# Optimization experiments

Hardware: AMD Instinct MI355X
Metric: run time of the kernel (lower is better)

Reference implementation:

```python
import jax, jax.numpy as jnp
import numpy as np

B, S, H, V = 256, 15, 512, 50257

def setup_inputs() -> dict:
    key = jax.random.key(0)
    ks = jax.random.split(key, 12)
    sc_h = 1.0 / np.sqrt(H)
    sc_in = 1.0 / np.sqrt(2 * H)
    return {
        "input_tokens": jax.random.randint(ks[0], (B, 1), 0, V),
        "hidden": jax.random.normal(ks[1], (1, B, H), jnp.float32),
        "encoder_outputs": jax.random.normal(ks[2], (B, S, H), jnp.float32),
        "emb_table": jax.random.normal(ks[3], (V, H), jnp.float32),
        "attn_W": jax.random.uniform(ks[4], (H, H), jnp.float32, -sc_h, sc_h),
        "attn_b": jax.random.uniform(ks[5], (H,), jnp.float32, -sc_h, sc_h),
        "W_ih": jax.random.uniform(ks[6], (3 * H, 2 * H), jnp.float32, -sc_in, sc_in),
        "W_hh": jax.random.uniform(ks[7], (3 * H, H), jnp.float32, -sc_h, sc_h),
        "b_ih": jax.random.uniform(ks[8], (3 * H,), jnp.float32, -sc_h, sc_h),
        "b_hh": jax.random.uniform(ks[9], (3 * H,), jnp.float32, -sc_h, sc_h),
        "out_W": jax.random.uniform(ks[10], (V, H), jnp.float32, -sc_h, sc_h),
        "out_b": jax.random.uniform(ks[11], (V,), jnp.float32, -sc_h, sc_h),
    }


def reference(input_tokens, hidden, encoder_outputs, emb_table, attn_W, attn_b,
              W_ih, W_hh, b_ih, b_hh, out_W, out_b):
    # Embedding (dropout is identity in eval/reference mode): [B,1,H]
    embedded = emb_table[input_tokens]
    h = hidden[0]  # [B,H]

    # Bahdanau-style scores, vectorized over the seq dim instead of the python loop:
    # energies[b,s] = attn(enc[b,s]);  score[b,s] = <h[b], energies[b,s]>
    energies = jnp.einsum("bsh,oh->bso", encoder_outputs, attn_W) + attn_b  # [B,S,H]
    attn_scores = jnp.einsum("bso,bo->bs", energies, h)                      # [B,S]
    attn_weights = jax.nn.softmax(attn_scores, axis=1)                       # [B,S]

    # context = weights @ encoder_outputs: [B,1,H]
    context = jnp.einsum("bs,bsh->bh", attn_weights, encoder_outputs)[:, None, :]

    # GRU single step (PyTorch gate order: r, z, n)
    x = jnp.concatenate([embedded, context], axis=2)[:, 0]  # [B,2H]
    gi = x @ W_ih.T + b_ih   # [B,3H]
    gh = h @ W_hh.T + b_hh   # [B,3H]
    i_r, i_z, i_n = jnp.split(gi, 3, axis=1)
    h_r, h_z, h_n = jnp.split(gh, 3, axis=1)
    r = jax.nn.sigmoid(i_r + h_r)
    z = jax.nn.sigmoid(i_z + h_z)
    n = jnp.tanh(i_n + r * h_n)
    h_new = (1.0 - z) * n + z * h            # [B,H]

    logits = h_new[:, None, :] @ out_W.T + out_b   # [B,1,V]
    log_probs = jax.nn.log_softmax(logits, axis=-1)
    return log_probs, h_new[None], attn_weights
```

## Files before the change

### kernel.cpp

```cpp
#include <hip/hip_runtime.h>

#define V_SIZE 50257
#define B_SIZE 256
#define S_LEN  15
#define H_DIM  512
#define NBLK_LG 786

typedef __attribute__((ext_vector_type(8))) short bf16x8;
typedef __attribute__((ext_vector_type(4))) float f32x4;

__device__ __forceinline__ unsigned short f2bf(float f) {
    unsigned int u = __float_as_uint(f);
    u += 0x7fffu + ((u >> 16) & 1u);
    return (unsigned short)(u >> 16);
}

__global__ __launch_bounds__(256) void attn_kernel(
    const float* __restrict__ hidden, const float* __restrict__ enc,
    const int* __restrict__ tokens, const float* __restrict__ emb,
    const float* __restrict__ attn_W, float* __restrict__ attnw_out,
    unsigned short* __restrict__ x_bf, unsigned short* __restrict__ h_bf)
{
    const int b = blockIdx.x, tid = threadIdx.x;
    __shared__ float e_s[S_LEN][H_DIM];
    __shared__ float h_sh[H_DIM];
    __shared__ float u_s[H_DIM];
    __shared__ float sc_s[S_LEN];
    __shared__ float w_s[S_LEN];
    {
        const float4* ev = (const float4*)(enc + (size_t)b * S_LEN * H_DIM);
        float4* es4 = (float4*)&e_s[0][0];
        #pragma unroll
        for (int i = 0; i < 8; ++i) {
            int idx = i * 256 + tid;
            if (idx < S_LEN * H_DIM / 4) es4[idx] = ev[idx];
        }
    }
    const float hv0 = hidden[(size_t)b * H_DIM + tid];
    const float hv1 = hidden[(size_t)b * H_DIM + tid + 256];
    h_sh[tid] = hv0; h_sh[tid + 256] = hv1;
    h_bf[(size_t)b * H_DIM + tid]       = f2bf(hv0);
    h_bf[(size_t)b * H_DIM + tid + 256] = f2bf(hv1);
    const int tok = tokens[b];
    x_bf[(size_t)b * 2 * H_DIM + tid]       = f2bf(emb[(size_t)tok * H_DIM + tid]);
    x_bf[(size_t)b * 2 * H_DIM + tid + 256] = f2bf(emb[(size_t)tok * H_DIM + tid + 256]);
    __syncthreads();
    {
        float u0 = 0.f, u1 = 0.f;
        #pragma unroll 8
        for (int o = 0; o < H_DIM; ++o) {
            const float hs = h_sh[o];
            u0 += hs * attn_W[(size_t)o * H_DIM + tid];
            u1 += hs * attn_W[(size_t)o * H_DIM + tid + 256];
        }
        u_s[tid] = u0; u_s[tid + 256] = u1;
    }
    __syncthreads();
    const int wave = tid >> 6, lane = tid & 63;
    for (int s = wave; s < S_LEN; s += 4) {
        float acc = 0.f;
        #pragma unroll
        for (int k = 0; k < H_DIM / 64; ++k)
            acc += e_s[s][lane + k * 64] * u_s[lane + k * 64];
        #pragma unroll
        for (int off = 32; off; off >>= 1) acc += __shfl_down(acc, off);
        if (lane == 0) sc_s[s] = acc;
    }
    __syncthreads();
    float mx = -1e30f;
    for (int s = 0; s < S_LEN; ++s) mx = fmaxf(mx, sc_s[s]);
    float sum = 0.f;
    for (int s = 0; s < S_LEN; ++s) sum += __expf(sc_s[s] - mx);
    const float inv = 1.f / sum;
    if (tid < S_LEN) {
        float w = __expf(sc_s[tid] - mx) * inv;
        w_s[tid] = w;
        attnw_out[b * S_LEN + tid] = w;
    }
    __syncthreads();
    #pragma unroll
    for (int hh = 0; hh < 2; ++hh) {
        int h = tid + hh * 256;
        float c = 0.f;
        #pragma unroll
        for (int s = 0; s < S_LEN; ++s)
            c += w_s[s] * e_s[s][h];
        x_bf[(size_t)b * 2 * H_DIM + H_DIM + h] = f2bf(c);
    }
}

struct GemmP {
    const unsigned short* A; const float* B; const float* bias; float* C;
    int N; int K;
};

template<int BM, int BN, int BK, int WR, int WC>
__global__ __launch_bounds__(256) void gemm_nt(GemmP p0, GemmP p1)
{
    GemmP p = (blockIdx.z == 0) ? p0 : p1;
    constexpr int LDA = BK + 8;
    __shared__ __align__(16) unsigned short As[BM][LDA];
    __shared__ __align__(16) unsigned short Bs[BN][LDA];
    const int tid = threadIdx.x;
    const int bn0 = blockIdx.x * BN;
    const int bm0 = blockIdx.y * BM;
    const int wave = tid >> 6, lane = tid & 63;
    const int wm = (wave / WC) * (BM / WR);
    const int wn = (wave % WC) * (BN / WC);
    constexpr int MF = BM / WR / 16, NF = BN / WC / 16;
    const int n16 = lane & 15, quad = lane >> 4;

    f32x4 acc[MF][NF] = {};

    for (int k0 = 0; k0 < p.K; k0 += BK) {
        #pragma unroll
        for (int it = 0; it < BM / 32; ++it) {
            int v = it * 256 + tid;
            int row = v >> 3, seg = v & 7;
            *(uint4*)&As[row][seg * 8] =
                *(const uint4*)(p.A + (size_t)(bm0 + row) * p.K + k0 + seg * 8);
        }
        #pragma unroll
        for (int it = 0; it < BN / 32; ++it) {
            int v = it * 256 + tid;
            int row = v >> 3, seg = v & 7;
            int gv = bn0 + row;
            float4 w0 = make_float4(0, 0, 0, 0), w1 = make_float4(0, 0, 0, 0);
            if (gv < p.N) {
                const float4* src = (const float4*)(p.B + (size_t)gv * p.K + k0 + seg * 8);
                w0 = src[0]; w1 = src[1];
            }
            uint4 pk;
            pk.x = (unsigned)f2bf(w0.x) | ((unsigned)f2bf(w0.y) << 16);
            pk.y = (unsigned)f2bf(w0.z) | ((unsigned)f2bf(w0.w) << 16);
            pk.z = (unsigned)f2bf(w1.x) | ((unsigned)f2bf(w1.y) << 16);
            pk.w = (unsigned)f2bf(w1.z) | ((unsigned)f2bf(w1.w) << 16);
            *(uint4*)&Bs[row][seg * 8] = pk;
        }
        __syncthreads();
        #pragma unroll
        for (int kk = 0; kk < BK; kk += 32) {
            bf16x8 af[MF], bfr[NF];
            #pragma unroll
            for (int i = 0; i < MF; ++i)
                af[i] = *(const bf16x8*)&As[wm + i * 16 + n16][kk + quad * 8];
            #pragma unroll
            for (int j = 0; j < NF; ++j)
                bfr[j] = *(const bf16x8*)&Bs[wn + j * 16 + n16][kk + quad * 8];
            #pragma unroll
            for (int i = 0; i < MF; ++i)
                #pragma unroll
                for (int j = 0; j < NF; ++j)
                    acc[i][j] = __builtin_amdgcn_mfma_f32_16x16x32_bf16(
                        af[i], bfr[j], acc[i][j], 0, 0, 0);
        }
        __syncthreads();
    }
    #pragma unroll
    for (int i = 0; i < MF; ++i) {
        const int r0 = bm0 + wm + i * 16 + quad * 4;
        #pragma unroll
        for (int j = 0; j < NF; ++j) {
            const int c = bn0 + wn + j * 16 + n16;
            if (c < p.N) {
                const float bv = p.bias[c];
                #pragma unroll
                for (int r = 0; r < 4; ++r)
                    p.C[(size_t)(r0 + r) * p.N + c] = acc[i][j][r] + bv;
            }
        }
    }
}

template<bool PART>
__global__ __launch_bounds__(256, 4) void gemm_lg(
    const unsigned short* __restrict__ A, const float* __restrict__ B,
    const float* __restrict__ bias, float* __restrict__ C,
    float* __restrict__ pm, float* __restrict__ ps, int bx0)
{
    constexpr int BN = 64, BK = 128;
    constexpr int LDB = BK + 8;
    __shared__ __align__(16) unsigned short Bs[BN][LDB];
    const int tid = threadIdx.x;
    const int blk = blockIdx.x;
    int bx, by;
    if (blk < 784) { int g = blk >> 4, s = blk & 15; bx = bx0 + g * 8 + (s & 7); by = s >> 3; }
    else           { int s = blk - 784;              bx = bx0 + 392;             by = s;      }
    const int bn0 = bx * BN;
    const int m0  = by * 128;
    const int wave = tid >> 6, lane = tid & 63;
    const int wm = wave * 32;
    const int n16 = lane & 15, quad = lane >> 4;

    f32x4 acc[2][4] = {};
    const unsigned short* arow[2];
    #pragma unroll
    for (int i = 0; i < 2; ++i)
        arow[i] = A + (size_t)(m0 + wm + i * 16 + n16) * H_DIM;

    for (int k0 = 0; k0 < H_DIM; k0 += BK) {
        #pragma unroll
        for (int it = 0; it < 4; ++it) {
            int v = it * 256 + tid;
            int row = v >> 4, seg = v & 15;
            int gv = bn0 + row;
            float4 w0 = make_float4(0, 0, 0, 0), w1 = make_float4(0, 0, 0, 0);
            if (gv < V_SIZE) {
                const float4* src = (const float4*)(B + (size_t)gv * H_DIM + k0 + seg * 8);
                w0 = src[0]; w1 = src[1];
            }
            uint4 pk;
            pk.x = (unsigned)f2bf(w0.x) | ((unsigned)f2bf(w0.y) << 16);
            pk.y = (unsigned)f2bf(w0.z) | ((unsigned)f2bf(w0.w) << 16);
            pk.z = (unsigned)f2bf(w1.x) | ((unsigned)f2bf(w1.y) << 16);
            pk.w = (unsigned)f2bf(w1.z) | ((unsigned)f2bf(w1.w) << 16);
            *(uint4*)&Bs[row][seg * 8] = pk;
        }
        __syncthreads();
        #pragma unroll
        for (int kk = 0; kk < BK; kk += 32) {
            bf16x8 af[2], bfr[4];
            #pragma unroll
            for (int i = 0; i < 2; ++i)
                af[i] = *(const bf16x8*)(arow[i] + k0 + kk + quad * 8);
            #pragma unroll
            for (int j = 0; j < 4; ++j)
                bfr[j] = *(const bf16x8*)&Bs[j * 16 + n16][kk + quad * 8];
            #pragma unroll
            for (int i = 0; i < 2; ++i)
                #pragma unroll
                for (int j = 0; j < 4; ++j)
                    acc[i][j] = __builtin_amdgcn_mfma_f32_16x16x32_bf16(
                        af[i], bfr[j], acc[i][j], 0, 0, 0);
        }
        __syncthreads();
    }

    int cj[4]; float bvv[4]; bool okj[4];
    #pragma unroll
    for (int j = 0; j < 4; ++j) {
        cj[j] = bn0 + j * 16 + n16;
        okj[j] = cj[j] < V_SIZE;
        bvv[j] = okj[j] ? bias[cj[j]] : 0.f;
    }
    #pragma unroll
    for (int i = 0; i < 2; ++i) {
        const int r0 = wm + i * 16 + quad * 4;
        if (PART) {
            #pragma unroll
            for (int r = 0; r < 4; ++r) {
                float m = -1e30f;
                #pragma unroll
                for (int j = 0; j < 4; ++j)
                    if (okj[j]) m = fmaxf(m, acc[i][j][r] + bvv[j]);
                #pragma unroll
                for (int d = 1; d < 16; d <<= 1) m = fmaxf(m, __shfl_xor(m, d));
                float s = 0.f;
                #pragma unroll
                for (int j = 0; j < 4; ++j)
                    if (okj[j]) s += __expf(acc[i][j][r] + bvv[j] - m);
                #pragma unroll
                for (int d = 1; d < 16; d <<= 1) s += __shfl_xor(s, d);
                if (n16 == 0) {
                    pm[(size_t)bx * B_SIZE + m0 + r0 + r] = m;
                    ps[(size_t)bx * B_SIZE + m0 + r0 + r] = s;
                }
            }
        }
        #pragma unroll
        for (int j = 0; j < 4; ++j) if (okj[j]) {
            #pragma unroll
            for (int r = 0; r < 4; ++r)
                C[(size_t)(m0 + r0 + r) * V_SIZE + cj[j]] = acc[i][j][r] + bvv[j];
        }
    }
}

__global__ __launch_bounds__(256) void gru_kernel(
    const float* __restrict__ gi, const float* __restrict__ gh,
    const float* __restrict__ hidden, float* __restrict__ hnew_out,
    unsigned short* __restrict__ hnew_bf)
{
    const int idx = blockIdx.x * 256 + threadIdx.x;
    const int b = idx >> 9, h = idx & 511;
    const float* gib = gi + (size_t)b * 3 * H_DIM;
    const float* ghb = gh + (size_t)b * 3 * H_DIM;
    float r = 1.f / (1.f + __expf(-(gib[h] + ghb[h])));
    float z = 1.f / (1.f + __expf(-(gib[H_DIM + h] + ghb[H_DIM + h])));
    float n = gib[2 * H_DIM + h] + r * ghb[2 * H_DIM + h];
    n = 1.f - 2.f / (1.f + __expf(2.f * n));
    float hp = hidden[idx];
    float hn = (1.f - z) * n + z * hp;
    hnew_out[idx] = hn;
    hnew_bf[idx] = f2bf(hn);
}

__global__ __launch_bounds__(1024) void finalize_kernel(
    float* __restrict__ logits, const float* __restrict__ pm,
    const float* __restrict__ ps)
{
    const int b = blockIdx.x, tid = threadIdx.x;
    float m = -1e30f, s = 0.f;
    for (int i = tid; i < NBLK_LG; i += 1024) {
        float mm = pm[(size_t)i * B_SIZE + b], ss = ps[(size_t)i * B_SIZE + b];
        float nm = fmaxf(m, mm);
        s = s * __expf(m - nm) + ss * __expf(mm - nm);
        m = nm;
    }
    const int lane = tid & 63, wave = tid >> 6;
    #pragma unroll
    for (int off = 32; off; off >>= 1) {
        float m2 = __shfl_down(m, off), s2 = __shfl_down(s, off);
        float nm = fmaxf(m, m2);
        s = s * __expf(m - nm) + s2 * __expf(m2 - nm);
        m = nm;
    }
    __shared__ float msh[16], ssh[16], lse_sh;
    if (lane == 0) { msh[wave] = m; ssh[wave] = s; }
    __syncthreads();
    if (tid == 0) {
        float M = msh[0], S = ssh[0];
        for (int w = 1; w < 16; ++w) {
            float nm = fmaxf(M, msh[w]);
            S = S * __expf(M - nm) + ssh[w] * __expf(msh[w] - nm);
            M = nm;
        }
        lse_sh = M + logf(S);
    }
    __syncthreads();
    const float lse = lse_sh;
    constexpr int HALF = 25132;
    const int start = blockIdx.y * HALF;
    const int end = min(V_SIZE, start + HALF);
    float* p0 = logits + (size_t)b * V_SIZE + start;
    const int n = end - start;
    const int mis = (int)(((uintptr_t)p0 >> 2) & 3);
    int pre = mis ? (4 - mis) : 0; if (pre > n) pre = n;
    if (tid < pre) p0[tid] -= lse;
    const int nvec = (n - pre) >> 2;
    float4* rv = (float4*)(p0 + pre);
    for (int i = tid; i < nvec; i += 1024) {
        float4 v = rv[i];
        v.x -= lse; v.y -= lse; v.z -= lse; v.w -= lse;
        rv[i] = v;
    }
    const int rem = n - pre - (nvec << 2);
    if (tid < rem) p0[pre + (nvec << 2) + tid] -= lse;
}

__global__ __launch_bounds__(1024) void logsoftmax_kernel(float* __restrict__ logits)
{
    const int b = blockIdx.x, tid = threadIdx.x;
    float* row = logits + (size_t)b * V_SIZE;
    float m = -1e30f, s = 0.f;
    for (int c = tid; c < V_SIZE; c += 1024) {
        float x = row[c];
        float nm = fmaxf(m, x);
        s = s * __expf(m - nm) + __expf(x - nm);
        m = nm;
    }
    const int lane = tid & 63, wave = tid >> 6;
    #pragma unroll
    for (int off = 32; off; off >>= 1) {
        float m2 = __shfl_down(m, off), s2 = __shfl_down(s, off);
        float nm = fmaxf(m, m2);
        s = s * __expf(m - nm) + s2 * __expf(m2 - nm);
        m = nm;
    }
    __shared__ float msh[16], ssh[16], lse_sh;
    if (lane == 0) { msh[wave] = m; ssh[wave] = s; }
    __syncthreads();
    if (tid == 0) {
        float M = msh[0], S = ssh[0];
        for (int w = 1; w < 16; ++w) {
            float nm = fmaxf(M, msh[w]);
            S = S * __expf(M - nm) + ssh[w] * __expf(msh[w] - nm);
            M = nm;
        }
        lse_sh = M + logf(S);
    }
    __syncthreads();
    const float lse = lse_sh;
    for (int c = tid; c < V_SIZE; c += 1024) row[c] -= lse;
}

constexpr size_t OFF_U      = 0;
constexpr size_t OFF_XBF    = 524288;
constexpr size_t OFF_HBF    = 1048576;
constexpr size_t OFF_HNEWBF = 1310720;
constexpr size_t OFF_GI     = 1572864;
constexpr size_t OFF_GH     = 3145728;
constexpr size_t OFF_PM     = 4718592;
constexpr size_t OFF_PS     = 5523456;
constexpr size_t WS_NEED    = 6328320;

extern "C" void kernel_launch(void* const* d_in, const int* in_sizes, int n_in,
                              void* d_out, int out_size, void* d_ws, size_t ws_size,
                              hipStream_t stream) {
    const int*   tokens = (const int*)d_in[0];
    const float* hidden = (const float*)d_in[1];
    const float* enc    = (const float*)d_in[2];
    const float* emb    = (const float*)d_in[3];
    const float* attn_W = (const float*)d_in[4];
    const float* W_ih   = (const float*)d_in[6];
    const float* W_hh   = (const float*)d_in[7];
    const float* b_ih   = (const float*)d_in[8];
    const float* b_hh   = (const float*)d_in[9];
    const float* out_W  = (const float*)d_in[10];
    const float* out_b  = (const float*)d_in[11];

    float* out = (float*)d_out;
    float* logp      = out;
    float* hnew_out  = out + (size_t)B_SIZE * V_SIZE;
    float* attnw_out = hnew_out + (size_t)B_SIZE * H_DIM;

    char* ws = (char*)d_ws;
    unsigned short* x_bf    = (unsigned short*)(ws + OFF_XBF);
    unsigned short* h_bf    = (unsigned short*)(ws + OFF_HBF);
    unsigned short* hnew_bf = (unsigned short*)(ws + OFF_HNEWBF);
    float*          gi_ws   = (float*)(ws + OFF_GI);
    float*          gh_ws   = (float*)(ws + OFF_GH);
    float*          pm_ws   = (float*)(ws + OFF_PM);
    float*          ps_ws   = (float*)(ws + OFF_PS);

    attn_kernel<<<dim3(256), 256, 0, stream>>>(hidden, enc, tokens, emb, attn_W,
                                               attnw_out, x_bf, h_bf);
    GemmP gi_p { x_bf, W_ih, b_ih, gi_ws, 3 * H_DIM, 2 * H_DIM };
    GemmP gh_p { h_bf, W_hh, b_hh, gh_ws, 3 * H_DIM, H_DIM };
    gemm_nt<64, 64, 64, 2, 2><<<dim3(24, 4, 2), 256, 0, stream>>>(gi_p, gh_p);
    gru_kernel<<<dim3(512), 256, 0, stream>>>(gi_ws, gh_ws, hidden, hnew_out, hnew_bf);

    if (ws_size >= WS_NEED) {
        gemm_lg<true><<<dim3(NBLK_LG), 256, 0, stream>>>(
            hnew_bf, out_W, out_b, logp, pm_ws, ps_ws, 0);
        gemm_lg<true><<<dim3(NBLK_LG), 256, 0, stream>>>(
            hnew_bf, out_W, out_b, logp, pm_ws, ps_ws, 393);
        finalize_kernel<<<dim3(256, 2), 1024, 0, stream>>>(logp, pm_ws, ps_ws);
    } else {
        gemm_lg<false><<<dim3(NBLK_LG), 256, 0, stream>>>(
            hnew_bf, out_W, out_b, logp, nullptr, nullptr, 0);
        gemm_lg<false><<<dim3(NBLK_LG), 256, 0, stream>>>(
            hnew_bf, out_W, out_b, logp, nullptr, nullptr, 393);
        logsoftmax_kernel<<<dim3(256), 1024, 0, stream>>>(logp);
    }
}
```

Before: 368.8 us.

## Double-buffer weight tiles in logits GEMM and merge into a single launch

The output-projection GEMM now prefetches the next K-slice of fp32 weights into registers while MFMAs run on the current shared-memory buffer, then converts it to bf16 into a second buffer. This replaces the load, sync, compute, sync sequence. The two half-vocabulary launches are also merged into one grid of 1572 blocks with remapped tile indexing, which saves a launch and its tail. In exchange, the kernel holds more registers for the prefetched values and uses twice the shared memory, which may lower occupancy under the 4-blocks-per-CU bound.

```diff
diff --git a/kernel.cpp b/kernel.cpp
--- a/kernel.cpp
+++ b/kernel.cpp
@@ -176,47 +176,64 @@
 __global__ __launch_bounds__(256, 4) void gemm_lg(
     const unsigned short* __restrict__ A, const float* __restrict__ B,
     const float* __restrict__ bias, float* __restrict__ C,
-    float* __restrict__ pm, float* __restrict__ ps, int bx0)
+    float* __restrict__ pm, float* __restrict__ ps)
 {
     constexpr int BN = 64, BK = 128;
     constexpr int LDB = BK + 8;
-    __shared__ __align__(16) unsigned short Bs[BN][LDB];
+    __shared__ __align__(16) unsigned short Bs[2][BN][LDB];
     const int tid = threadIdx.x;
     const int blk = blockIdx.x;
     int bx, by;
-    if (blk < 784) { int g = blk >> 4, s = blk & 15; bx = bx0 + g * 8 + (s & 7); by = s >> 3; }
-    else           { int s = blk - 784;              bx = bx0 + 392;             by = s;      }
+    if (blk < 1568) { int g = blk >> 4, s = blk & 15; bx = g * 8 + (s & 7); by = s >> 3; }
+    else            { int s = blk - 1568;             bx = 784 + (s >> 1);  by = s & 1;  }
     const int bn0 = bx * BN;
     const int m0  = by * 128;
     const int wave = tid >> 6, lane = tid & 63;
     const int wm = wave * 32;
     const int n16 = lane & 15, quad = lane >> 4;
 
+    const int srow_base = tid >> 4;
+    const int sseg = tid & 15;
+
+    float4 r0[4], r1[4];
+    auto LOAD = [&](int k0) {
+        #pragma unroll
+        for (int it = 0; it < 4; ++it) {
+            int gv = bn0 + it * 16 + srow_base;
+            if (gv < V_SIZE) {
+                const float4* src = (const float4*)(B + (size_t)gv * H_DIM + k0 + sseg * 8);
+                r0[it] = src[0]; r1[it] = src[1];
+            } else {
+                r0[it] = make_float4(0, 0, 0, 0); r1[it] = make_float4(0, 0, 0, 0);
+            }
+        }
+    };
+    auto CVTW = [&](int buf) {
+        #pragma unroll
+        for (int it = 0; it < 4; ++it) {
+            uint4 pk;
+            pk.x = (unsigned)f2bf(r0[it].x) | ((unsigned)f2bf(r0[it].y) << 16);
+            pk.y = (unsigned)f2bf(r0[it].z) | ((unsigned)f2bf(r0[it].w) << 16);
+            pk.z = (unsigned)f2bf(r1[it].x) | ((unsigned)f2bf(r1[it].y) << 16);
+            pk.w = (unsigned)f2bf(r1[it].z) | ((unsigned)f2bf(r1[it].w) << 16);
+            *(uint4*)&Bs[buf][it * 16 + srow_base][sseg * 8] = pk;
+        }
+    };
+
     f32x4 acc[2][4] = {};
     const unsigned short* arow[2];
     #pragma unroll
     for (int i = 0; i < 2; ++i)
         arow[i] = A + (size_t)(m0 + wm + i * 16 + n16) * H_DIM;
 
-    for (int k0 = 0; k0 < H_DIM; k0 += BK) {
-        #pragma unroll
-        for (int it = 0; it < 4; ++it) {
-            int v = it * 256 + tid;
-            int row = v >> 4, seg = v & 15;
-            int gv = bn0 + row;
-            float4 w0 = make_float4(0, 0, 0, 0), w1 = make_float4(0, 0, 0, 0);
-            if (gv < V_SIZE) {
-                const float4* src = (const float4*)(B + (size_t)gv * H_DIM + k0 + seg * 8);
-                w0 = src[0]; w1 = src[1];
-            }
-            uint4 pk;
-            pk.x = (unsigned)f2bf(w0.x) | ((unsigned)f2bf(w0.y) << 16);
-            pk.y = (unsigned)f2bf(w0.z) | ((unsigned)f2bf(w0.w) << 16);
-            pk.z = (unsigned)f2bf(w1.x) | ((unsigned)f2bf(w1.y) << 16);
-            pk.w = (unsigned)f2bf(w1.z) | ((unsigned)f2bf(w1.w) << 16);
-            *(uint4*)&Bs[row][seg * 8] = pk;
-        }
-        __syncthreads();
+    LOAD(0);
+    CVTW(0);
+    __syncthreads();
+
+    #pragma unroll
+    for (int t = 0; t < 4; ++t) {
+        const int k0 = t * BK;
+        if (t < 3) LOAD(k0 + BK);
         #pragma unroll
         for (int kk = 0; kk < BK; kk += 32) {
             bf16x8 af[2], bfr[4];
@@ -225,7 +242,7 @@
                 af[i] = *(const bf16x8*)(arow[i] + k0 + kk + quad * 8);
             #pragma unroll
             for (int j = 0; j < 4; ++j)
-                bfr[j] = *(const bf16x8*)&Bs[j * 16 + n16][kk + quad * 8];
+                bfr[j] = *(const bf16x8*)&Bs[t & 1][j * 16 + n16][kk + quad * 8];
             #pragma unroll
             for (int i = 0; i < 2; ++i)
                 #pragma unroll
@@ -233,7 +250,10 @@
                     acc[i][j] = __builtin_amdgcn_mfma_f32_16x16x32_bf16(
                         af[i], bfr[j], acc[i][j], 0, 0, 0);
         }
-        __syncthreads();
+        if (t < 3) {
+            CVTW((t + 1) & 1);
+            __syncthreads();
+        }
     }
 
     int cj[4]; float bvv[4]; bool okj[4];
@@ -245,7 +265,7 @@
     }
     #pragma unroll
     for (int i = 0; i < 2; ++i) {
-        const int r0 = wm + i * 16 + quad * 4;
+        const int r0i = wm + i * 16 + quad * 4;
         if (PART) {
             #pragma unroll
             for (int r = 0; r < 4; ++r) {
@@ -262,8 +282,8 @@
                 #pragma unroll
                 for (int d = 1; d < 16; d <<= 1) s += __shfl_xor(s, d);
                 if (n16 == 0) {
-                    pm[(size_t)bx * B_SIZE + m0 + r0 + r] = m;
-                    ps[(size_t)bx * B_SIZE + m0 + r0 + r] = s;
+                    pm[(size_t)bx * B_SIZE + m0 + r0i + r] = m;
+                    ps[(size_t)bx * B_SIZE + m0 + r0i + r] = s;
                 }
             }
         }
@@ -271,7 +291,7 @@
         for (int j = 0; j < 4; ++j) if (okj[j]) {
             #pragma unroll
             for (int r = 0; r < 4; ++r)
-                C[(size_t)(m0 + r0 + r) * V_SIZE + cj[j]] = acc[i][j][r] + bvv[j];
+                C[(size_t)(m0 + r0i + r) * V_SIZE + cj[j]] = acc[i][j][r] + bvv[j];
         }
     }
 }
@@ -384,7 +404,6 @@
     for (int c = tid; c < V_SIZE; c += 1024) row[c] -= lse;
 }
 
-constexpr size_t OFF_U      = 0;
 constexpr size_t OFF_XBF    = 524288;
 constexpr size_t OFF_HBF    = 1048576;
 constexpr size_t OFF_HNEWBF = 1310720;
@@ -431,16 +450,12 @@
     gru_kernel<<<dim3(512), 256, 0, stream>>>(gi_ws, gh_ws, hidden, hnew_out, hnew_bf);
 
     if (ws_size >= WS_NEED) {
-        gemm_lg<true><<<dim3(NBLK_LG), 256, 0, stream>>>(
-            hnew_bf, out_W, out_b, logp, pm_ws, ps_ws, 0);
-        gemm_lg<true><<<dim3(NBLK_LG), 256, 0, stream>>>(
-            hnew_bf, out_W, out_b, logp, pm_ws, ps_ws, 393);
+        gemm_lg<true><<<dim3(2 * NBLK_LG), 256, 0, stream>>>(
+            hnew_bf, out_W, out_b, logp, pm_ws, ps_ws);
         finalize_kernel<<<dim3(256, 2), 1024, 0, stream>>>(logp, pm_ws, ps_ws);
     } else {
-        gemm_lg<false><<<dim3(NBLK_LG), 256, 0, stream>>>(
-            hnew_bf, out_W, out_b, logp, nullptr, nullptr, 0);
-        gemm_lg<false><<<dim3(NBLK_LG), 256, 0, stream>>>(
-            hnew_bf, out_W, out_b, logp, nullptr, nullptr, 393);
+        gemm_lg<false><<<dim3(2 * NBLK_LG), 256, 0, stream>>>(
+            hnew_bf, out_W, out_b, logp, nullptr, nullptr);
         logsoftmax_kernel<<<dim3(256), 1024, 0, stream>>>(logp);
     }
 }
```

Result: faster. 359.1 us (-2.6%).
